# Kernel optimization log

Hardware: AMD Instinct MI355X
Metric: run time of the kernel (lower is better)

The kernel has to match this reference:

```python
import jax, jax.numpy as jnp
import numpy as np


def setup_inputs() -> dict:
    key = jax.random.key(0)
    k1, k2, k3 = jax.random.split(key, 3)
    B, C, H, W = 16, 256, 80, 80
    MED, K = 128, 128
    x = jax.random.normal(k1, (B, C, H, W), dtype=jnp.float32)
    w1 = jax.random.normal(k2, (MED, C), dtype=jnp.float32) * 0.05
    b1 = jnp.zeros((MED,), dtype=jnp.float32)
    w2 = jax.random.normal(k3, (C, MED), dtype=jnp.float32) * 0.05
    b2 = jnp.zeros((C,), dtype=jnp.float32)
    return {"x": x, "w1": w1, "b1": b1, "w2": w2, "b2": b2, "out_c": K}


def reference(x, w1, b1, w2, b2, out_c):
    # 1x1 conv MLP: in_c -> med_c -> in_c (pointwise GEMMs)
    h = jnp.einsum('bchw,mc->bmhw', x, w1) + b1[None, :, None, None]
    x_ = jnp.einsum('bmhw,cm->bchw', h, w2) + b2[None, :, None, None]
    xs = jax.nn.sigmoid(x_)
    # per-pixel top-k over channels: work in NHWC so channel is last axis
    xs_t = jnp.transpose(xs, (0, 2, 3, 1))              # [B,H,W,C]
    _, xi = jax.lax.top_k(xs_t, out_c)                  # [B,H,W,K]
    x_t = jnp.transpose(x, (0, 2, 3, 1))                # [B,H,W,C]
    xl_t = jnp.transpose(x_, (0, 2, 3, 1))              # [B,H,W,C]
    out1 = jnp.take_along_axis(x_t, xi, axis=-1)        # [B,H,W,K]
    out2 = jnp.take_along_axis(xl_t, xi, axis=-1)       # [B,H,W,K]
    return jnp.transpose(out1 * out2, (0, 3, 1, 2))     # [B,K,H,W]
```

## Files before the change

### kernel.cpp

```cpp
#include <hip/hip_runtime.h>
#include <math.h>

#define CIN  256
#define MEDC 128
#define KOUT 128
#define HWSZ 6400
#define NB   16
#define TP   16
#define SROW 272

typedef unsigned int u32;
typedef unsigned long long u64;

__device__ __forceinline__ float numpy_expf(float x) {
#pragma clang fp contract(off)
    const float q = __builtin_rintf(x * 1.44269504088896341f);
    float r = __builtin_fmaf(q, -0.693359375f, x);
    r = __builtin_fmaf(q, 2.12194440e-4f, r);
    float p = __builtin_fmaf(1.9875691500e-4f, r, 1.3981999507e-3f);
    p = __builtin_fmaf(p, r, 8.3334519073e-3f);
    p = __builtin_fmaf(p, r, 4.1665795894e-2f);
    p = __builtin_fmaf(p, r, 1.6666665459e-1f);
    p = __builtin_fmaf(p, r, 5.0000001201e-1f);
    const float r2 = r * r;
    p = __builtin_fmaf(p, r2, r);
    p = p + 1.0f;
    return __builtin_ldexpf(p, (int)q);
}

__global__ void prep_T(const float* __restrict__ w1, const float* __restrict__ w2,
                       float* __restrict__ w1t, float* __restrict__ w2t) {
    const int c = blockIdx.x;
    const int m = threadIdx.x;
    w1t[c * MEDC + m] = w1[m * CIN + c];
    const int q  = c & 63;
    const int ci = c >> 6;
    w2t[m * CIN + q * 4 + ci] = w2[c * MEDC + m];
}


template<int D, int STAGE>
__device__ __forceinline__ void intra_ct(u64 (&k)[16]) {
#pragma unroll
    for (int r = 0; r < 16; ++r) {
        if (!(r & D)) {
            const bool dsc = (r >> STAGE) & 1;
            const bool sw  = (k[r] > k[r ^ D]) != dsc;
            const u64 x0 = k[r], x1 = k[r ^ D];
            k[r]     = sw ? x1 : x0;
            k[r ^ D] = sw ? x0 : x1;
        }
    }
}

template<int D>
__device__ __forceinline__ void intra_rt(u64 (&k)[16], const bool dsc) {
#pragma unroll
    for (int r = 0; r < 16; ++r) {
        if (!(r & D)) {
            const bool sw = (k[r] > k[r ^ D]) != dsc;
            const u64 x0 = k[r], x1 = k[r ^ D];
            k[r]     = sw ? x1 : x0;
            k[r ^ D] = sw ? x0 : x1;
        }
    }
}

template<int SWZ>
__device__ __forceinline__ u64 swz64(u64 v) {
    const int lo = __builtin_amdgcn_ds_swizzle((int)(unsigned)v, SWZ);
    const int hi = __builtin_amdgcn_ds_swizzle((int)(unsigned)(v >> 32), SWZ);
    return ((u64)(unsigned)hi << 32) | (u64)(unsigned)lo;
}

template<int M, int SWZ>
__device__ __forceinline__ void cross_rt(u64 (&k)[16], const int l16, const bool dsc) {
    const bool keepmax = ((l16 & M) != 0) != dsc;
#pragma unroll
    for (int r = 0; r < 16; ++r) {
        const u64 other = swz64<SWZ>(k[r]);
        const bool gt = k[r] > other;
        k[r] = (gt == keepmax) ? k[r] : other;
    }
}

__global__ __launch_bounds__(256, 4)
void csel_main(const float* __restrict__ x,
               const float* __restrict__ w1t, const float* __restrict__ w2t,
               const float* __restrict__ b1, const float* __restrict__ b2,
               float* __restrict__ out) {
    __shared__ __align__(16) float xs[CIN * 20];
    __shared__ __align__(16) u32 s_arr[TP * SROW];
    float* hs = (float*)s_arr;

    const int t    = threadIdx.x;
    const int pix0 = blockIdx.x * TP;
    const int b    = pix0 / HWSZ;
    const int hw0  = pix0 % HWSZ;
    const float* xb = x + (size_t)b * CIN * HWSZ + hw0;

    {
        const int p  = t & (TP - 1);
        const int c0 = t >> 4;
        #pragma unroll
        for (int i = 0; i < 16; ++i) {
            const int c = c0 + i * 16;
            xs[c * 20 + p] = xb[(size_t)c * HWSZ + p];
        }
    }
    __syncthreads();

    const int ml = (t & 63) * 2;
    const int pg = t >> 6;
    float a1[2][4] = {{0.f,0.f,0.f,0.f},{0.f,0.f,0.f,0.f}};

    #pragma unroll 4
    for (int c = 0; c < CIN; ++c) {
        const float2 wv = *(const float2*)&w1t[c * MEDC + ml];
        const float4 xv = *(const float4*)&xs[c * 20 + pg * 4];
        a1[0][0] = fmaf(wv.x, xv.x, a1[0][0]);
        a1[0][1] = fmaf(wv.x, xv.y, a1[0][1]);
        a1[0][2] = fmaf(wv.x, xv.z, a1[0][2]);
        a1[0][3] = fmaf(wv.x, xv.w, a1[0][3]);
        a1[1][0] = fmaf(wv.y, xv.x, a1[1][0]);
        a1[1][1] = fmaf(wv.y, xv.y, a1[1][1]);
        a1[1][2] = fmaf(wv.y, xv.z, a1[1][2]);
        a1[1][3] = fmaf(wv.y, xv.w, a1[1][3]);
    }
    #pragma unroll
    for (int i = 0; i < 2; ++i) {
        const float bi = b1[ml + i];
        #pragma unroll
        for (int j = 0; j < 4; ++j)
            hs[(ml + i) * 20 + pg * 4 + j] = a1[i][j] + bi;
    }
    __syncthreads();

    const int q  = t & 63;
    const int p0 = (t >> 6) * 4;
    float a2[4][4];
    #pragma unroll
    for (int i = 0; i < 4; ++i)
        #pragma unroll
        for (int j = 0; j < 4; ++j) a2[i][j] = 0.f;

    #pragma unroll 2
    for (int m = 0; m < MEDC; ++m) {
        const float4 wv = *(const float4*)&w2t[m * CIN + q * 4];
        const float4 hv = *(const float4*)&hs[m * 20 + p0];
        a2[0][0] = fmaf(wv.x, hv.x, a2[0][0]);
        a2[0][1] = fmaf(wv.x, hv.y, a2[0][1]);
        a2[0][2] = fmaf(wv.x, hv.z, a2[0][2]);
        a2[0][3] = fmaf(wv.x, hv.w, a2[0][3]);
        a2[1][0] = fmaf(wv.y, hv.x, a2[1][0]);
        a2[1][1] = fmaf(wv.y, hv.y, a2[1][1]);
        a2[1][2] = fmaf(wv.y, hv.z, a2[1][2]);
        a2[1][3] = fmaf(wv.y, hv.w, a2[1][3]);
        a2[2][0] = fmaf(wv.z, hv.x, a2[2][0]);
        a2[2][1] = fmaf(wv.z, hv.y, a2[2][1]);
        a2[2][2] = fmaf(wv.z, hv.z, a2[2][2]);
        a2[2][3] = fmaf(wv.z, hv.w, a2[2][3]);
        a2[3][0] = fmaf(wv.w, hv.x, a2[3][0]);
        a2[3][1] = fmaf(wv.w, hv.y, a2[3][1]);
        a2[3][2] = fmaf(wv.w, hv.z, a2[3][2]);
        a2[3][3] = fmaf(wv.w, hv.w, a2[3][3]);
    }
    float xv32[4][4];
    #pragma unroll
    for (int ci = 0; ci < 4; ++ci) {
        const float bi = b2[q + 64 * ci];
        #pragma unroll
        for (int pj = 0; pj < 4; ++pj)
            xv32[ci][pj] = a2[ci][pj] + bi;
    }
    __syncthreads();

    #pragma unroll
    for (int ci = 0; ci < 4; ++ci) {
        const int c    = q + 64 * ci;
        const int slot = c + (c >> 4);
        #pragma unroll
        for (int pj = 0; pj < 4; ++pj) {
#pragma clang fp contract(off)
            const int p2 = p0 + pj;
            const float e  = numpy_expf(-xv32[ci][pj]);
            const float dd = 1.0f + e;
            const float s  = 1.0f / dd;
            s_arr[p2 * SROW + slot] = __float_as_uint(s);
            xs[c * 20 + p2] = xs[c * 20 + p2] * xv32[ci][pj];
        }
    }
    __syncthreads();

    const int p   = t >> 4;
    const int l16 = t & 15;

    u64 k[16];
    {
        const u32* sp = &s_arr[p * SROW + l16 * 17];
        const int cbase = l16 * 16;
        #pragma unroll
        for (int r = 0; r < 16; ++r) {
            const u64 s = (u64)sp[r];
            k[r] = (s << 8) | (u64)(255 - (cbase + r));
        }
    }

    intra_ct<1, 1>(k);
    intra_ct<2, 2>(k); intra_ct<1, 2>(k);
    intra_ct<4, 3>(k); intra_ct<2, 3>(k); intra_ct<1, 3>(k);
    {
        const bool dsc = (l16 & 1) != 0;
        intra_rt<8>(k, dsc); intra_rt<4>(k, dsc); intra_rt<2>(k, dsc); intra_rt<1>(k, dsc);
    }
    {
        const bool dsc = ((l16 >> 1) & 1) != 0;
        cross_rt<1, 0x041F>(k, l16, dsc);
        intra_rt<8>(k, dsc); intra_rt<4>(k, dsc); intra_rt<2>(k, dsc); intra_rt<1>(k, dsc);
    }
    {
        const bool dsc = ((l16 >> 2) & 1) != 0;
        cross_rt<2, 0x081F>(k, l16, dsc);
        cross_rt<1, 0x041F>(k, l16, dsc);
        intra_rt<8>(k, dsc); intra_rt<4>(k, dsc); intra_rt<2>(k, dsc); intra_rt<1>(k, dsc);
    }
    {
        const bool dsc = ((l16 >> 3) & 1) != 0;
        cross_rt<4, 0x101F>(k, l16, dsc);
        cross_rt<2, 0x081F>(k, l16, dsc);
        cross_rt<1, 0x041F>(k, l16, dsc);
        intra_rt<8>(k, dsc); intra_rt<4>(k, dsc); intra_rt<2>(k, dsc); intra_rt<1>(k, dsc);
    }
    {
        cross_rt<8, 0x201F>(k, l16, false);
        cross_rt<4, 0x101F>(k, l16, false);
        cross_rt<2, 0x081F>(k, l16, false);
        cross_rt<1, 0x041F>(k, l16, false);
        intra_rt<8>(k, false); intra_rt<4>(k, false); intra_rt<2>(k, false); intra_rt<1>(k, false);
    }

    if (l16 >= 8) {
        const int rbase = 255 - l16 * 16;
        float* ob = out + (size_t)b * KOUT * HWSZ + hw0 + p;
        #pragma unroll
        for (int r = 0; r < 16; ++r) {
            const int c = 255 - (int)(k[r] & 0xFF);
            ob[(size_t)(rbase - r) * HWSZ] = xs[c * 20 + p];
        }
    }
}

extern "C" void kernel_launch(void* const* d_in, const int* in_sizes, int n_in,
                              void* d_out, int out_size, void* d_ws, size_t ws_size,
                              hipStream_t stream) {
    const float* x  = (const float*)d_in[0];
    const float* w1 = (const float*)d_in[1];
    const float* b1 = (const float*)d_in[2];
    const float* w2 = (const float*)d_in[3];
    const float* b2 = (const float*)d_in[4];

    float* w1t = (float*)d_ws;
    float* w2t = w1t + CIN * MEDC;

    prep_T<<<CIN, MEDC, 0, stream>>>(w1, w2, w1t, w2t);
    csel_main<<<(NB * HWSZ) / TP, 256, 0, stream>>>(x, w1t, w2t, b1, b2, (float*)d_out);
}
```

Before: 520.5 us.

## Keep hidden activations in registers and broadcast via readlane in second GEMM

The intermediate hidden tile is no longer written to shared memory. Each wave keeps its own 4-pixel slice of h in registers, and the second GEMM broadcasts each hidden value across the wave with readlane. This removes the shared-memory store, one barrier and the per-iteration LDS reads of h. W2 loads go through an 8-deep register ring buffer so global latency is prefetched. The cost is a fully unrolled 128-iteration loop with many readlane (scalar) operations and higher register pressure, which could lower occupancy.

```diff
diff --git a/kernel.cpp b/kernel.cpp
--- a/kernel.cpp
+++ b/kernel.cpp
@@ -91,7 +91,6 @@
                float* __restrict__ out) {
     __shared__ __align__(16) float xs[CIN * 20];
     __shared__ __align__(16) u32 s_arr[TP * SROW];
-    float* hs = (float*)s_arr;
 
     const int t    = threadIdx.x;
     const int pix0 = blockIdx.x * TP;
@@ -110,14 +109,17 @@
     }
     __syncthreads();
 
-    const int ml = (t & 63) * 2;
-    const int pg = t >> 6;
+    const int lw = t & 63;
+    const int wq = t >> 6;
+    const int ml = lw * 2;
+    const float b1a = b1[ml];
+    const float b1b = b1[ml + 1];
     float a1[2][4] = {{0.f,0.f,0.f,0.f},{0.f,0.f,0.f,0.f}};
 
     #pragma unroll 4
     for (int c = 0; c < CIN; ++c) {
         const float2 wv = *(const float2*)&w1t[c * MEDC + ml];
-        const float4 xv = *(const float4*)&xs[c * 20 + pg * 4];
+        const float4 xv = *(const float4*)&xs[c * 20 + wq * 4];
         a1[0][0] = fmaf(wv.x, xv.x, a1[0][0]);
         a1[0][1] = fmaf(wv.x, xv.y, a1[0][1]);
         a1[0][2] = fmaf(wv.x, xv.z, a1[0][2]);
@@ -127,62 +129,77 @@
         a1[1][2] = fmaf(wv.y, xv.z, a1[1][2]);
         a1[1][3] = fmaf(wv.y, xv.w, a1[1][3]);
     }
-    #pragma unroll
-    for (int i = 0; i < 2; ++i) {
-        const float bi = b1[ml + i];
-        #pragma unroll
-        for (int j = 0; j < 4; ++j)
-            hs[(ml + i) * 20 + pg * 4 + j] = a1[i][j] + bi;
+    float h8[8];
+    #pragma unroll
+    for (int j = 0; j < 4; ++j) {
+        h8[j]     = a1[0][j] + b1a;
+        h8[4 + j] = a1[1][j] + b1b;
+    }
+
+    const float b2v0 = b2[lw];
+    const float b2v1 = b2[lw + 64];
+    const float b2v2 = b2[lw + 128];
+    const float b2v3 = b2[lw + 192];
+    const float* w2p = w2t + lw * 4;
+
+    float4 wbuf[8];
+    #pragma unroll
+    for (int m0 = 0; m0 < 8; ++m0)
+        wbuf[m0] = *(const float4*)&w2p[m0 * CIN];
+
+    float a2[4][4];
+    #pragma unroll
+    for (int i = 0; i < 4; ++i)
+        #pragma unroll
+        for (int j = 0; j < 4; ++j) a2[i][j] = 0.f;
+
+    #pragma unroll
+    for (int m = 0; m < MEDC; ++m) {
+        const float4 wv = wbuf[m & 7];
+        float hb[4];
+        #pragma unroll
+        for (int pj = 0; pj < 4; ++pj) {
+            const int reg = (m & 1) * 4 + pj;
+            hb[pj] = __int_as_float(
+                __builtin_amdgcn_readlane(__float_as_int(h8[reg]), m >> 1));
+        }
+        a2[0][0] = fmaf(wv.x, hb[0], a2[0][0]);
+        a2[0][1] = fmaf(wv.x, hb[1], a2[0][1]);
+        a2[0][2] = fmaf(wv.x, hb[2], a2[0][2]);
+        a2[0][3] = fmaf(wv.x, hb[3], a2[0][3]);
+        a2[1][0] = fmaf(wv.y, hb[0], a2[1][0]);
+        a2[1][1] = fmaf(wv.y, hb[1], a2[1][1]);
+        a2[1][2] = fmaf(wv.y, hb[2], a2[1][2]);
+        a2[1][3] = fmaf(wv.y, hb[3], a2[1][3]);
+        a2[2][0] = fmaf(wv.z, hb[0], a2[2][0]);
+        a2[2][1] = fmaf(wv.z, hb[1], a2[2][1]);
+        a2[2][2] = fmaf(wv.z, hb[2], a2[2][2]);
+        a2[2][3] = fmaf(wv.z, hb[3], a2[2][3]);
+        a2[3][0] = fmaf(wv.w, hb[0], a2[3][0]);
+        a2[3][1] = fmaf(wv.w, hb[1], a2[3][1]);
+        a2[3][2] = fmaf(wv.w, hb[2], a2[3][2]);
+        a2[3][3] = fmaf(wv.w, hb[3], a2[3][3]);
+        if (m + 8 < MEDC)
+            wbuf[m & 7] = *(const float4*)&w2p[(m + 8) * CIN];
+    }
+    float xv32[4][4];
+    #pragma unroll
+    for (int pj = 0; pj < 4; ++pj) {
+        xv32[0][pj] = a2[0][pj] + b2v0;
+        xv32[1][pj] = a2[1][pj] + b2v1;
+        xv32[2][pj] = a2[2][pj] + b2v2;
+        xv32[3][pj] = a2[3][pj] + b2v3;
     }
     __syncthreads();
 
-    const int q  = t & 63;
-    const int p0 = (t >> 6) * 4;
-    float a2[4][4];
-    #pragma unroll
-    for (int i = 0; i < 4; ++i)
-        #pragma unroll
-        for (int j = 0; j < 4; ++j) a2[i][j] = 0.f;
-
-    #pragma unroll 2
-    for (int m = 0; m < MEDC; ++m) {
-        const float4 wv = *(const float4*)&w2t[m * CIN + q * 4];
-        const float4 hv = *(const float4*)&hs[m * 20 + p0];
-        a2[0][0] = fmaf(wv.x, hv.x, a2[0][0]);
-        a2[0][1] = fmaf(wv.x, hv.y, a2[0][1]);
-        a2[0][2] = fmaf(wv.x, hv.z, a2[0][2]);
-        a2[0][3] = fmaf(wv.x, hv.w, a2[0][3]);
-        a2[1][0] = fmaf(wv.y, hv.x, a2[1][0]);
-        a2[1][1] = fmaf(wv.y, hv.y, a2[1][1]);
-        a2[1][2] = fmaf(wv.y, hv.z, a2[1][2]);
-        a2[1][3] = fmaf(wv.y, hv.w, a2[1][3]);
-        a2[2][0] = fmaf(wv.z, hv.x, a2[2][0]);
-        a2[2][1] = fmaf(wv.z, hv.y, a2[2][1]);
-        a2[2][2] = fmaf(wv.z, hv.z, a2[2][2]);
-        a2[2][3] = fmaf(wv.z, hv.w, a2[2][3]);
-        a2[3][0] = fmaf(wv.w, hv.x, a2[3][0]);
-        a2[3][1] = fmaf(wv.w, hv.y, a2[3][1]);
-        a2[3][2] = fmaf(wv.w, hv.z, a2[3][2]);
-        a2[3][3] = fmaf(wv.w, hv.w, a2[3][3]);
-    }
-    float xv32[4][4];
     #pragma unroll
     for (int ci = 0; ci < 4; ++ci) {
-        const float bi = b2[q + 64 * ci];
-        #pragma unroll
-        for (int pj = 0; pj < 4; ++pj)
-            xv32[ci][pj] = a2[ci][pj] + bi;
-    }
-    __syncthreads();
-
-    #pragma unroll
-    for (int ci = 0; ci < 4; ++ci) {
-        const int c    = q + 64 * ci;
+        const int c    = lw + 64 * ci;
         const int slot = c + (c >> 4);
         #pragma unroll
         for (int pj = 0; pj < 4; ++pj) {
 #pragma clang fp contract(off)
-            const int p2 = p0 + pj;
+            const int p2 = wq * 4 + pj;
             const float e  = numpy_expf(-xv32[ci][pj]);
             const float dd = 1.0f + e;
             const float s  = 1.0f / dd;
```

Measured after the change: 504.0 us. -3.2%, faster.
